# Kernel optimization log

Hardware: AMD Instinct MI355X
Metric: run time of the kernel (lower is better)

## Reference

```python
import jax, jax.numpy as jnp
import numpy as np

F_NODE = 256   # node_feat_size
H      = 256   # hidden_size (must equal F_NODE due to expand using feat_size)
M      = 128   # max_child_num
T      = 4     # edge_type_num
ITERS  = 2     # num_iterations
NSEM   = 57    # Tree.num_sem


def setup_inputs() -> dict:
    key = jax.random.key(0)
    ks = jax.random.split(key, 12)

    def lin(k, fan_in, shape):
        return jax.random.normal(k, shape, jnp.float32) / np.sqrt(fan_in).astype(np.float32)

    return dict(
        parent_feature=jax.random.normal(ks[0], (1, F_NODE), jnp.float32),
        gt_children_code=jax.random.normal(ks[1], (1, 16), jnp.float32),
        gt_num_code=jax.random.normal(ks[2], (1, 10), jnp.float32),
        W_parent=lin(ks[3], F_NODE + 26, (F_NODE + 26, H * M)),
        b_parent=jnp.zeros((H * M,), jnp.float32),
        W_exists=lin(ks[4], H, (H, 1)),
        b_exists=jnp.zeros((1,), jnp.float32),
        W_sem=lin(ks[5], H, (H, NSEM)),
        b_sem=jnp.zeros((NSEM,), jnp.float32),
        W_el=lin(ks[6], 2 * H, (2 * H, H)),
        b_el=jnp.zeros((H,), jnp.float32),
        W_ee=lin(ks[7], H, (T, H)),          # stacked per-type [H,1] heads
        b_ee=jnp.zeros((T,), jnp.float32),
        W_ne=lin(ks[8], 3 * H + T, (ITERS, 3 * H + T, H)),
        b_ne=jnp.zeros((ITERS, H), jnp.float32),
        W_child=lin(ks[9], (ITERS + 1) * H, ((ITERS + 1) * H, H)),
        b_child=jnp.zeros((H,), jnp.float32),
        W_child2=lin(ks[10], H, (H, F_NODE)),
        b_child2=jnp.zeros((F_NODE,), jnp.float32),
    )


def reference(parent_feature, gt_children_code, gt_num_code,
              W_parent, b_parent, W_exists, b_exists, W_sem, b_sem,
              W_el, b_el, W_ee, b_ee, W_ne, b_ne,
              W_child, b_child, W_child2, b_child2):
    B = parent_feature.shape[0]  # == 1 (message passing uses batch index 0 only)

    pf = jnp.concatenate([parent_feature, gt_children_code, gt_num_code], axis=1)
    child_feats = jax.nn.relu(pf @ W_parent + b_parent).reshape(B, M, H)

    child_exists_logits = child_feats @ W_exists + b_exists           # [B,M,1]

    # pairwise edge latents [B,M,M,H]
    pair = jnp.concatenate([
        jnp.broadcast_to(child_feats[:, :, None, :], (B, M, M, H)),
        jnp.broadcast_to(child_feats[:, None, :, :], (B, M, M, H)),
    ], axis=3)
    edge_latents = jax.nn.relu(pair @ W_el + b_el)                    # [B,M,M,H]
    edge_exists_logits = jnp.einsum('bijh,th->bijt', edge_latents, W_ee) + b_ee  # [B,M,M,T]

    # --- masked full candidate edge set (replaces data-dependent torch.nonzero) ---
    ii, jj, tt = jnp.meshgrid(jnp.arange(M), jnp.arange(M), jnp.arange(T), indexing='ij')
    i = ii.reshape(-1)   # [E] source nodes
    j = jj.reshape(-1)
    t = tt.reshape(-1)

    logit_e = edge_exists_logits[0].reshape(-1)                        # [E], same (i,j,t) order
    exists0 = child_exists_logits[0, :, 0] > 0                         # [M]
    mask = (logit_e > 0) & exists0[i] & exists0[j]                     # [E]
    maskf = mask.astype(child_feats.dtype)[:, None]

    edge_feats_mp = edge_latents[0][i, j]                              # [E,H]
    edge_type_logit = jax.nn.one_hot(t, T, dtype=logit_e.dtype) * logit_e[:, None]  # [E,T]
    ef = jnp.concatenate([edge_feats_mp, edge_type_logit], axis=1)     # [E,H+T]

    cf0 = child_feats[0]                                               # [M,H]
    iter_feats = [cf0]
    for it in range(ITERS):
        x = jnp.concatenate([cf0[i], cf0[j], ef], axis=1)              # [E,3H+T]
        msg = jax.nn.relu(x @ W_ne[it] + b_ne[it]) * maskf             # masked msgs are 0
        # scatter_max with zero-initialized out (relu msgs >= 0, matches torch_scatter out=zeros)
        cf0 = jnp.zeros((M, H), msg.dtype).at[i].max(msg)
        iter_feats.append(cf0)

    all_feats = jnp.concatenate(iter_feats, axis=1)                    # [M,(ITERS+1)H]
    h = jax.nn.relu(all_feats @ W_child + b_child)                     # [M,H]
    child_sem_logits = (h @ W_sem + b_sem)[None]                       # [1,M,NSEM]
    child_out = jax.nn.relu(h @ W_child2 + b_child2)[None]             # [1,M,F_NODE]
    return (child_out, child_sem_logits, child_exists_logits, edge_exists_logits)
```

## Files before the change

kernel.cpp:

```cpp
#include <hip/hip_runtime.h>
#include <hip/hip_bf16.h>
#include <stdint.h>


typedef unsigned short ushort_t;
using f32x4 = __attribute__((ext_vector_type(4))) float;
using s16x8 = __attribute__((ext_vector_type(8))) short;

__device__ __forceinline__ ushort_t f2bf(float x) {
  __hip_bfloat16 h = __float2bfloat16(x);
  return *reinterpret_cast<ushort_t*>(&h);
}

__global__ __launch_bounds__(256) void k1_parent(
    const float* __restrict__ p0, const float* __restrict__ p1, const float* __restrict__ p2,
    const float* __restrict__ W, const float* __restrict__ b, float* __restrict__ cf) {
  __shared__ float pfs[282];
  __shared__ f32x4 red[320];
  int tid = threadIdx.x;
  pfs[tid] = p0[tid];
  if (tid < 16) pfs[256 + tid] = p1[tid];
  if (tid < 10) pfs[272 + tid] = p2[tid];
  __syncthreads();
  int c = tid & 7, s = tid >> 3;
  int colg = blockIdx.x * 8 + c;
  const f32x4* W4 = (const f32x4*)W;
  int k0 = (s * 282) >> 5, k1e = ((s + 1) * 282) >> 5;
  f32x4 acc = {0.f, 0.f, 0.f, 0.f};
  #pragma unroll 4
  for (int k = k0; k < k1e; ++k)
    acc += pfs[k] * W4[(size_t)k * 8192 + colg];
  red[s * 8 + c] = acc;
  __syncthreads();
  if (tid < 64) {
    int col = tid & 7, part = tid >> 3;
    f32x4 v = red[(part * 4 + 0) * 8 + col] + red[(part * 4 + 1) * 8 + col]
            + red[(part * 4 + 2) * 8 + col] + red[(part * 4 + 3) * 8 + col];
    red[256 + part * 8 + col] = v;
  }
  __syncthreads();
  if (tid < 8) {
    f32x4 v = red[256 + tid];
    #pragma unroll
    for (int q = 1; q < 8; ++q) v += red[256 + q * 8 + tid];
    v += ((const f32x4*)b)[blockIdx.x * 8 + tid];
    #pragma unroll
    for (int q = 0; q < 4; ++q) v[q] = fmaxf(v[q], 0.f);
    ((f32x4*)cf)[blockIdx.x * 8 + tid] = v;
  }
}

__global__ __launch_bounds__(1024) void ks1(
    const float* __restrict__ cf, const float* __restrict__ Wel,
    const float* __restrict__ Wne, const float* __restrict__ bne,
    const float* __restrict__ Wex, const float* __restrict__ bex,
    float* __restrict__ A, float* __restrict__ B, float* __restrict__ P,
    float* __restrict__ Q, float* __restrict__ ex0, float* __restrict__ exout,
    ushort_t* __restrict__ W3T) {
  __shared__ float c[256];
  __shared__ float redA[1024], redB[1024], redP[1024], redQ[1024];
  __shared__ float wsum[4];
  int tid = threadIdx.x;
  int r = blockIdx.x >> 1, half = blockIdx.x & 1;
  if (tid < 256) c[tid] = cf[r * 256 + tid];
  __syncthreads();
  int cc = tid & 127, s = tid >> 7;
  int col = half * 128 + cc;
  int k0 = s * 32;
  const float* WelB = Wel + 256 * 256;
  float aA = 0.f, aB = 0.f, aP = 0.f, aQ = 0.f;
  #pragma unroll 4
  for (int kk = 0; kk < 32; ++kk) {
    int k = k0 + kk;
    float cv = c[k];
    aA += cv * Wel[k * 256 + col];
    aB += cv * WelB[k * 256 + col];
    aP += cv * Wne[k * 256 + col];
    aQ += cv * Wne[(256 + k) * 256 + col];
  }
  redA[tid] = aA; redB[tid] = aB; redP[tid] = aP; redQ[tid] = aQ;
  float v = (half == 0 && tid < 256) ? c[tid] * Wex[tid] : 0.f;
  #pragma unroll
  for (int off = 32; off; off >>= 1) v += __shfl_xor(v, off);
  if (half == 0 && tid < 256 && (tid & 63) == 0) wsum[tid >> 6] = v;
  __syncthreads();
  if (tid < 128) {
    int cl = half * 128 + tid;
    float a = 0.f, bb = 0.f, pv = bne[cl], qv = 0.f;
    #pragma unroll
    for (int q = 0; q < 8; ++q) {
      a  += redA[q * 128 + tid];
      bb += redB[q * 128 + tid];
      pv += redP[q * 128 + tid];
      qv += redQ[q * 128 + tid];
    }
    A[r * 256 + cl] = a;
    B[r * 256 + cl] = bb;
    P[r * 256 + cl] = pv;
    Q[r * 256 + cl] = qv;
  }
  if (half == 0 && tid == 0) {
    float lg = wsum[0] + wsum[1] + wsum[2] + wsum[3] + bex[0];
    exout[r] = lg;
    ex0[r] = lg > 0.f ? 1.f : 0.f;
  }
  if (tid < 512) {
    int idx = blockIdx.x * 512 + tid;
    int it = idx >> 16, n = (idx >> 8) & 255, k = idx & 255;
    W3T[it * 65536 + n * 256 + (k ^ ((n & 7) << 3))] =
        f2bf(Wne[(size_t)(it * 772 + 512 + k) * 256 + n]);
  }
}

__global__ __launch_bounds__(256) void k3_edge(
    const float* __restrict__ A, const float* __restrict__ B, const float* __restrict__ bel,
    const float* __restrict__ Wee, const float* __restrict__ bee,
    ushort_t* __restrict__ ELbf, float* __restrict__ elog) {
  __shared__ float w4s[4][4][4];
  int tid = threadIdx.x, lane = tid & 63, wid = tid >> 6;
  int p0 = blockIdx.x * 4;
  int i = p0 >> 7;
  float a = A[i * 256 + tid] + bel[tid];
  float we0 = Wee[tid], we1 = Wee[256 + tid], we2 = Wee[512 + tid], we3 = Wee[768 + tid];
  #pragma unroll
  for (int jj = 0; jj < 4; ++jj) {
    int pr = p0 + jj;
    int j = pr & 127;
    float el = fmaxf(a + B[j * 256 + tid], 0.f);
    ELbf[(size_t)pr * 256 + (tid ^ ((pr & 7) << 3))] = f2bf(el);
    float t0 = el * we0, t1 = el * we1, t2 = el * we2, t3 = el * we3;
    #pragma unroll
    for (int off = 32; off; off >>= 1) {
      t0 += __shfl_xor(t0, off);
      t1 += __shfl_xor(t1, off);
      t2 += __shfl_xor(t2, off);
      t3 += __shfl_xor(t3, off);
    }
    if (lane == 0) { w4s[jj][wid][0] = t0; w4s[jj][wid][1] = t1;
                     w4s[jj][wid][2] = t2; w4s[jj][wid][3] = t3; }
  }
  __syncthreads();
  if (tid < 16) {
    int jj = tid >> 2, t = tid & 3;
    float v = w4s[jj][0][t] + w4s[jj][1][t] + w4s[jj][2][t] + w4s[jj][3][t] + bee[t];
    elog[(p0 + jj) * 4 + t] = v;
  }
}

__global__ __launch_bounds__(512) void kf(
    const ushort_t* __restrict__ ELbf, const ushort_t* __restrict__ W3T_it,
    const float* __restrict__ Wne_it, const float* __restrict__ P,
    const float* __restrict__ Q, const float* __restrict__ ex0,
    const float* __restrict__ elog, float* __restrict__ cfn) {
  __shared__ __align__(16) ushort_t lA[128 * 256];
  __shared__ __align__(16) ushort_t lB[128 * 256];
  __shared__ float sl[512];
  __shared__ float se[128];
  __shared__ float red[256];
  int tid = threadIdx.x;
  int i = blockIdx.x >> 1, nh = blockIdx.x & 1;
  if (ex0[i] == 0.f) {
    if (tid < 128) cfn[i * 256 + nh * 128 + tid] = 0.f;
    return;
  }
  int lane = tid & 63, wid = tid >> 6;
  int wr = wid >> 2, wc = wid & 3;
  sl[tid] = elog[i * 512 + tid];
  if (tid < 128) se[tid] = ex0[tid];
  float pv = (tid < 128) ? P[i * 256 + nh * 128 + tid] : 0.f;
  float qv[2][16];
  float w4v[2][4];
  #pragma unroll
  for (int nt = 0; nt < 2; ++nt) {
    int col = nh * 128 + wc * 32 + nt * 16 + (lane & 15);
    #pragma unroll
    for (int t = 0; t < 4; ++t) w4v[nt][t] = Wne_it[(768 + t) * 256 + col];
    #pragma unroll
    for (int mt = 0; mt < 4; ++mt)
      #pragma unroll
      for (int r = 0; r < 4; ++r) {
        int j = wr * 64 + mt * 16 + (lane >> 4) * 4 + r;
        qv[nt][mt * 4 + r] = Q[j * 256 + col];
      }
  }
  #pragma unroll
  for (int rr = 0; rr < 8; ++rr) {
    int c = rr * 8 + wid;
    const ushort_t* sa = ELbf + (size_t)(i * 128) * 256 + c * 512 + lane * 8;
    const ushort_t* sb = W3T_it + (size_t)(nh * 128) * 256 + c * 512 + lane * 8;
    __builtin_amdgcn_global_load_lds((const __attribute__((address_space(1))) void*)sa,
                                     (__attribute__((address_space(3))) void*)(lA + c * 512), 16, 0, 0);
    __builtin_amdgcn_global_load_lds((const __attribute__((address_space(1))) void*)sb,
                                     (__attribute__((address_space(3))) void*)(lB + c * 512), 16, 0, 0);
  }
  __syncthreads();
  f32x4 acc[4][2] = {};
  #pragma unroll
  for (int ks = 0; ks < 8; ++ks) {
    s16x8 af[4], bfr[2];
    #pragma unroll
    for (int mt = 0; mt < 4; ++mt) {
      int row = wr * 64 + mt * 16 + (lane & 15);
      int kl = (ks * 32 + (lane >> 4) * 8) ^ ((row & 7) << 3);
      af[mt] = *reinterpret_cast<const s16x8*>(&lA[row * 256 + kl]);
    }
    #pragma unroll
    for (int nt = 0; nt < 2; ++nt) {
      int n = wc * 32 + nt * 16 + (lane & 15);
      int kl = (ks * 32 + (lane >> 4) * 8) ^ ((n & 7) << 3);
      bfr[nt] = *reinterpret_cast<const s16x8*>(&lB[n * 256 + kl]);
    }
    #pragma unroll
    for (int mt = 0; mt < 4; ++mt)
      #pragma unroll
      for (int nt = 0; nt < 2; ++nt)
        acc[mt][nt] = __builtin_amdgcn_mfma_f32_16x16x32_bf16(af[mt], bfr[nt], acc[mt][nt], 0, 0, 0);
  }
  const float NEG = -3.0e38f;
  #pragma unroll
  for (int nt = 0; nt < 2; ++nt) {
    float mx = NEG;
    #pragma unroll
    for (int mt = 0; mt < 4; ++mt)
      #pragma unroll
      for (int r = 0; r < 4; ++r) {
        int j = wr * 64 + mt * 16 + (lane >> 4) * 4 + r;
        float base = acc[mt][nt][r] + qv[nt][mt * 4 + r];
        if (se[j] > 0.f) {
          float l0 = sl[j * 4 + 0], l1 = sl[j * 4 + 1];
          float l2 = sl[j * 4 + 2], l3 = sl[j * 4 + 3];
          if (l0 > 0.f) mx = fmaxf(mx, base + l0 * w4v[nt][0]);
          if (l1 > 0.f) mx = fmaxf(mx, base + l1 * w4v[nt][1]);
          if (l2 > 0.f) mx = fmaxf(mx, base + l2 * w4v[nt][2]);
          if (l3 > 0.f) mx = fmaxf(mx, base + l3 * w4v[nt][3]);
        }
      }
    mx = fmaxf(mx, __shfl_xor(mx, 16));
    mx = fmaxf(mx, __shfl_xor(mx, 32));
    if (lane < 16) red[wr * 128 + wc * 32 + nt * 16 + lane] = mx;
  }
  __syncthreads();
  if (tid < 128) {
    float m = fmaxf(red[tid], red[128 + tid]);
    cfn[i * 256 + nh * 128 + tid] = fmaxf(pv + m, 0.f);
  }
}

__global__ __launch_bounds__(1024) void kp1(
    const float* __restrict__ cf, const float* __restrict__ Wne_it,
    const float* __restrict__ bne_it, float* __restrict__ P, float* __restrict__ Q) {
  __shared__ float c[256];
  __shared__ float redP[1024], redQ[1024];
  int tid = threadIdx.x;
  int r = blockIdx.x >> 1, half = blockIdx.x & 1;
  if (tid < 256) c[tid] = cf[r * 256 + tid];
  __syncthreads();
  int cc = tid & 127, s = tid >> 7;
  int col = half * 128 + cc;
  int k0 = s * 32;
  float aP = 0.f, aQ = 0.f;
  #pragma unroll 4
  for (int kk = 0; kk < 32; ++kk) {
    int k = k0 + kk;
    float cv = c[k];
    aP += cv * Wne_it[k * 256 + col];
    aQ += cv * Wne_it[(256 + k) * 256 + col];
  }
  redP[tid] = aP; redQ[tid] = aQ;
  __syncthreads();
  if (tid < 128) {
    int cl = half * 128 + tid;
    float pv = bne_it[cl], qv = 0.f;
    #pragma unroll
    for (int q = 0; q < 8; ++q) { pv += redP[q * 128 + tid]; qv += redQ[q * 128 + tid]; }
    P[r * 256 + cl] = pv;
    Q[r * 256 + cl] = qv;
  }
}

__global__ __launch_bounds__(1024) void k6_final(
    const float* __restrict__ cf0, const float* __restrict__ cf1, const float* __restrict__ cf2,
    const float* __restrict__ Wc, const float* __restrict__ bc,
    const float* __restrict__ Wsem, const float* __restrict__ bsem,
    const float* __restrict__ W2, const float* __restrict__ b2,
    float* __restrict__ out) {
  __shared__ float af[768];
  __shared__ float red[1024];
  __shared__ float hrow[256];
  __shared__ float redS[8 * 57];
  int tid = threadIdx.x;
  int m = blockIdx.x >> 1, half = blockIdx.x & 1;
  if (tid < 768) {
    af[tid] = tid < 256 ? cf0[m * 256 + tid]
            : tid < 512 ? cf1[m * 256 + tid - 256]
                        : cf2[m * 256 + tid - 512];
  }
  __syncthreads();
  {
    int cc = tid & 255, s = tid >> 8;
    float acc = 0.f;
    #pragma unroll 4
    for (int kk = 0; kk < 192; ++kk) {
      int k = s * 192 + kk;
      acc += af[k] * Wc[k * 256 + cc];
    }
    red[tid] = acc;
  }
  __syncthreads();
  if (tid < 256) {
    float v = bc[tid] + red[tid] + red[256 + tid] + red[512 + tid] + red[768 + tid];
    hrow[tid] = fmaxf(v, 0.f);
  }
  __syncthreads();
  int cc = tid & 127, s = tid >> 7;
  int col = half * 128 + cc;
  {
    float acc = 0.f;
    #pragma unroll 4
    for (int kk = 0; kk < 32; ++kk) {
      int k = s * 32 + kk;
      acc += hrow[k] * W2[k * 256 + col];
    }
    red[tid] = acc;
    if (half == 0 && cc < 57) {
      float accs = 0.f;
      #pragma unroll 4
      for (int kk = 0; kk < 32; ++kk) {
        int k = s * 32 + kk;
        accs += hrow[k] * Wsem[k * 57 + cc];
      }
      redS[s * 57 + cc] = accs;
    }
  }
  __syncthreads();
  if (tid < 128) {
    float v = b2[half * 128 + tid];
    #pragma unroll
    for (int q = 0; q < 8; ++q) v += red[q * 128 + tid];
    out[m * 256 + half * 128 + tid] = fmaxf(v, 0.f);
  }
  if (half == 0 && tid < 57) {
    float v = bsem[tid];
    #pragma unroll
    for (int q = 0; q < 8; ++q) v += redS[q * 57 + tid];
    out[32768 + m * 57 + tid] = v;
  }
}

extern "C" void kernel_launch(void* const* d_in, const int* in_sizes, int n_in,
                              void* d_out, int out_size, void* d_ws, size_t ws_size,
                              hipStream_t stream) {
  const float* p0  = (const float*)d_in[0];
  const float* p1  = (const float*)d_in[1];
  const float* p2  = (const float*)d_in[2];
  const float* Wp  = (const float*)d_in[3];
  const float* bp  = (const float*)d_in[4];
  const float* Wex = (const float*)d_in[5];
  const float* bex = (const float*)d_in[6];
  const float* Wsm = (const float*)d_in[7];
  const float* bsm = (const float*)d_in[8];
  const float* Wel = (const float*)d_in[9];
  const float* bel = (const float*)d_in[10];
  const float* Wee = (const float*)d_in[11];
  const float* bee = (const float*)d_in[12];
  const float* Wne = (const float*)d_in[13];
  const float* bne = (const float*)d_in[14];
  const float* Wc  = (const float*)d_in[15];
  const float* bc  = (const float*)d_in[16];
  const float* W2  = (const float*)d_in[17];
  const float* b2  = (const float*)d_in[18];
  float* out = (float*)d_out;

  char* ws = (char*)d_ws;
  float*    cf0  = (float*)(ws + 0);
  float*    cf1  = (float*)(ws + 131072);
  float*    cf2  = (float*)(ws + 262144);
  float*    Ab   = (float*)(ws + 393216);
  float*    Bb   = (float*)(ws + 524288);
  float*    Pb   = (float*)(ws + 655360);
  float*    Qb   = (float*)(ws + 786432);
  float*    Pb2  = (float*)(ws + 917504);
  float*    Qb2  = (float*)(ws + 1048576);
  float*    ex0  = (float*)(ws + 1179648);
  ushort_t* W3T  = (ushort_t*)(ws + 1310720);
  ushort_t* ELbf = (ushort_t*)(ws + 2097152);

  float* out_ex = out + 40064;
  float* out_el = out + 40192;

  const float* Wne1 = Wne + 772 * 256;

  k1_parent<<<1024, 256, 0, stream>>>(p0, p1, p2, Wp, bp, cf0);
  ks1<<<256, 1024, 0, stream>>>(cf0, Wel, Wne, bne, Wex, bex,
                                Ab, Bb, Pb, Qb, ex0, out_ex, W3T);
  k3_edge<<<4096, 256, 0, stream>>>(Ab, Bb, bel, Wee, bee, ELbf, out_el);
  kf<<<256, 512, 0, stream>>>(ELbf, W3T, Wne, Pb, Qb, ex0, out_el, cf1);
  kp1<<<256, 1024, 0, stream>>>(cf1, Wne1, bne + 256, Pb2, Qb2);
  kf<<<256, 512, 0, stream>>>(ELbf, W3T + 65536, Wne1, Pb2, Qb2, ex0, out_el, cf2);
  k6_final<<<256, 1024, 0, stream>>>(cf0, cf1, cf2, Wc, bc, Wsm, bsm, W2, b2, out);
}
```

Baseline: 187.8 us.

## Fuse edge-latent computation into message-passing GEMM kernel, recompute per iteration

Drops the separate edge kernel and its bf16 edge-latent buffer in global memory. Each message-passing block now builds its 128x256 edge-latent tile directly in LDS from the A row, the B matrix and the bias. The first iteration's instance also computes the edge-type logits and writes them out. This removes a launch and a write/read round trip of the pairwise tensor, at the cost of recomputing the tile in both iterations and in both column-half blocks, plus extra LDS and global reads of B per block.

```diff
diff --git a/kernel.cpp b/kernel.cpp
--- a/kernel.cpp
+++ b/kernel.cpp
@@ -112,88 +112,107 @@
   }
 }
 
-__global__ __launch_bounds__(256) void k3_edge(
-    const float* __restrict__ A, const float* __restrict__ B, const float* __restrict__ bel,
-    const float* __restrict__ Wee, const float* __restrict__ bee,
-    ushort_t* __restrict__ ELbf, float* __restrict__ elog) {
-  __shared__ float w4s[4][4][4];
-  int tid = threadIdx.x, lane = tid & 63, wid = tid >> 6;
-  int p0 = blockIdx.x * 4;
-  int i = p0 >> 7;
-  float a = A[i * 256 + tid] + bel[tid];
-  float we0 = Wee[tid], we1 = Wee[256 + tid], we2 = Wee[512 + tid], we3 = Wee[768 + tid];
-  #pragma unroll
-  for (int jj = 0; jj < 4; ++jj) {
-    int pr = p0 + jj;
-    int j = pr & 127;
-    float el = fmaxf(a + B[j * 256 + tid], 0.f);
-    ELbf[(size_t)pr * 256 + (tid ^ ((pr & 7) << 3))] = f2bf(el);
-    float t0 = el * we0, t1 = el * we1, t2 = el * we2, t3 = el * we3;
-    #pragma unroll
-    for (int off = 32; off; off >>= 1) {
-      t0 += __shfl_xor(t0, off);
-      t1 += __shfl_xor(t1, off);
-      t2 += __shfl_xor(t2, off);
-      t3 += __shfl_xor(t3, off);
-    }
-    if (lane == 0) { w4s[jj][wid][0] = t0; w4s[jj][wid][1] = t1;
-                     w4s[jj][wid][2] = t2; w4s[jj][wid][3] = t3; }
-  }
-  __syncthreads();
-  if (tid < 16) {
-    int jj = tid >> 2, t = tid & 3;
-    float v = w4s[jj][0][t] + w4s[jj][1][t] + w4s[jj][2][t] + w4s[jj][3][t] + bee[t];
-    elog[(p0 + jj) * 4 + t] = v;
-  }
-}
-
-__global__ __launch_bounds__(512) void kf(
-    const ushort_t* __restrict__ ELbf, const ushort_t* __restrict__ W3T_it,
+template<int WRITE_EL>
+__global__ __launch_bounds__(512) void kf2(
+    const float* __restrict__ A, const float* __restrict__ Bm,
+    const float* __restrict__ bel, const float* __restrict__ Wee,
+    const float* __restrict__ bee, const ushort_t* __restrict__ W3T_it,
     const float* __restrict__ Wne_it, const float* __restrict__ P,
     const float* __restrict__ Q, const float* __restrict__ ex0,
-    const float* __restrict__ elog, float* __restrict__ cfn) {
+    float* __restrict__ elog, float* __restrict__ cfn) {
   __shared__ __align__(16) ushort_t lA[128 * 256];
   __shared__ __align__(16) ushort_t lB[128 * 256];
+  __shared__ float arow[256], belr[256];
+  __shared__ float weer[1024];
   __shared__ float sl[512];
   __shared__ float se[128];
   __shared__ float red[256];
   int tid = threadIdx.x;
   int i = blockIdx.x >> 1, nh = blockIdx.x & 1;
-  if (ex0[i] == 0.f) {
+  bool alive = ex0[i] != 0.f;
+  if (!alive && (WRITE_EL == 0 || nh == 1)) {
     if (tid < 128) cfn[i * 256 + nh * 128 + tid] = 0.f;
     return;
   }
   int lane = tid & 63, wid = tid >> 6;
   int wr = wid >> 2, wc = wid & 3;
-  sl[tid] = elog[i * 512 + tid];
+  if (alive) {
+    #pragma unroll
+    for (int rr = 0; rr < 8; ++rr) {
+      int ch = rr * 8 + wid;
+      const ushort_t* sb = W3T_it + (size_t)(nh * 128) * 256 + ch * 512 + lane * 8;
+      __builtin_amdgcn_global_load_lds((const __attribute__((address_space(1))) void*)sb,
+                                       (__attribute__((address_space(3))) void*)(lB + ch * 512), 16, 0, 0);
+    }
+  }
+  if (tid < 256) { arow[tid] = A[i * 256 + tid]; belr[tid] = bel[tid]; }
   if (tid < 128) se[tid] = ex0[tid];
-  float pv = (tid < 128) ? P[i * 256 + nh * 128 + tid] : 0.f;
+  if (WRITE_EL) { weer[tid] = Wee[tid]; weer[512 + tid] = Wee[512 + tid]; }
+  else sl[tid] = elog[i * 512 + tid];
+  float pv = 0.f;
   float qv[2][16];
   float w4v[2][4];
+  if (alive) {
+    pv = (tid < 128) ? P[i * 256 + nh * 128 + tid] : 0.f;
+    #pragma unroll
+    for (int nt = 0; nt < 2; ++nt) {
+      int col = nh * 128 + wc * 32 + nt * 16 + (lane & 15);
+      #pragma unroll
+      for (int t = 0; t < 4; ++t) w4v[nt][t] = Wne_it[(768 + t) * 256 + col];
+      #pragma unroll
+      for (int mt = 0; mt < 4; ++mt)
+        #pragma unroll
+        for (int r = 0; r < 4; ++r)
+          qv[nt][mt * 4 + r] = Q[(wr * 64 + mt * 16 + (lane >> 4) * 4 + r) * 256 + col];
+    }
+  }
+  __syncthreads();
+  int j = tid >> 2, q = tid & 3;
+  int sw = (j & 7) << 3;
+  float lg0 = 0.f, lg1 = 0.f, lg2 = 0.f, lg3 = 0.f;
+  const float* Bj = Bm + j * 256;
   #pragma unroll
-  for (int nt = 0; nt < 2; ++nt) {
-    int col = nh * 128 + wc * 32 + nt * 16 + (lane & 15);
-    #pragma unroll
-    for (int t = 0; t < 4; ++t) w4v[nt][t] = Wne_it[(768 + t) * 256 + col];
-    #pragma unroll
-    for (int mt = 0; mt < 4; ++mt)
+  for (int ch = 0; ch < 8; ++ch) {
+    int c0 = q * 64 + ch * 8;
+    float el[8];
+    #pragma unroll
+    for (int e = 0; e < 8; ++e)
+      el[e] = fmaxf(arow[c0 + e] + Bj[c0 + e] + belr[c0 + e], 0.f);
+    if (WRITE_EL) {
       #pragma unroll
-      for (int r = 0; r < 4; ++r) {
-        int j = wr * 64 + mt * 16 + (lane >> 4) * 4 + r;
-        qv[nt][mt * 4 + r] = Q[j * 256 + col];
+      for (int e = 0; e < 8; ++e) {
+        lg0 += el[e] * weer[c0 + e];
+        lg1 += el[e] * weer[256 + c0 + e];
+        lg2 += el[e] * weer[512 + c0 + e];
+        lg3 += el[e] * weer[768 + c0 + e];
       }
-  }
-  #pragma unroll
-  for (int rr = 0; rr < 8; ++rr) {
-    int c = rr * 8 + wid;
-    const ushort_t* sa = ELbf + (size_t)(i * 128) * 256 + c * 512 + lane * 8;
-    const ushort_t* sb = W3T_it + (size_t)(nh * 128) * 256 + c * 512 + lane * 8;
-    __builtin_amdgcn_global_load_lds((const __attribute__((address_space(1))) void*)sa,
-                                     (__attribute__((address_space(3))) void*)(lA + c * 512), 16, 0, 0);
-    __builtin_amdgcn_global_load_lds((const __attribute__((address_space(1))) void*)sb,
-                                     (__attribute__((address_space(3))) void*)(lB + c * 512), 16, 0, 0);
-  }
-  __syncthreads();
+    }
+    s16x8 sv;
+    #pragma unroll
+    for (int e = 0; e < 8; ++e) sv[e] = (short)f2bf(el[e]);
+    *reinterpret_cast<s16x8*>(&lA[j * 256 + (c0 ^ sw)]) = sv;
+  }
+  if (WRITE_EL) {
+    lg0 += __shfl_xor(lg0, 1); lg0 += __shfl_xor(lg0, 2);
+    lg1 += __shfl_xor(lg1, 1); lg1 += __shfl_xor(lg1, 2);
+    lg2 += __shfl_xor(lg2, 1); lg2 += __shfl_xor(lg2, 2);
+    lg3 += __shfl_xor(lg3, 1); lg3 += __shfl_xor(lg3, 2);
+    if (q == 0) {
+      float v0 = lg0 + bee[0], v1 = lg1 + bee[1], v2 = lg2 + bee[2], v3 = lg3 + bee[3];
+      sl[j * 4 + 0] = v0; sl[j * 4 + 1] = v1; sl[j * 4 + 2] = v2; sl[j * 4 + 3] = v3;
+      if (nh == 0) {
+        elog[(i * 128 + j) * 4 + 0] = v0;
+        elog[(i * 128 + j) * 4 + 1] = v1;
+        elog[(i * 128 + j) * 4 + 2] = v2;
+        elog[(i * 128 + j) * 4 + 3] = v3;
+      }
+    }
+  }
+  __syncthreads();
+  if (!alive) {
+    if (tid < 128) cfn[i * 256 + tid] = 0.f;
+    return;
+  }
   f32x4 acc[4][2] = {};
   #pragma unroll
   for (int ks = 0; ks < 8; ++ks) {
@@ -224,11 +243,11 @@
     for (int mt = 0; mt < 4; ++mt)
       #pragma unroll
       for (int r = 0; r < 4; ++r) {
-        int j = wr * 64 + mt * 16 + (lane >> 4) * 4 + r;
+        int jj = wr * 64 + mt * 16 + (lane >> 4) * 4 + r;
         float base = acc[mt][nt][r] + qv[nt][mt * 4 + r];
-        if (se[j] > 0.f) {
-          float l0 = sl[j * 4 + 0], l1 = sl[j * 4 + 1];
-          float l2 = sl[j * 4 + 2], l3 = sl[j * 4 + 3];
+        if (se[jj] > 0.f) {
+          float l0 = sl[jj * 4 + 0], l1 = sl[jj * 4 + 1];
+          float l2 = sl[jj * 4 + 2], l3 = sl[jj * 4 + 3];
           if (l0 > 0.f) mx = fmaxf(mx, base + l0 * w4v[nt][0]);
           if (l1 > 0.f) mx = fmaxf(mx, base + l1 * w4v[nt][1]);
           if (l2 > 0.f) mx = fmaxf(mx, base + l2 * w4v[nt][2]);
@@ -383,7 +402,6 @@
   float*    Qb2  = (float*)(ws + 1048576);
   float*    ex0  = (float*)(ws + 1179648);
   ushort_t* W3T  = (ushort_t*)(ws + 1310720);
-  ushort_t* ELbf = (ushort_t*)(ws + 2097152);
 
   float* out_ex = out + 40064;
   float* out_el = out + 40192;
@@ -393,9 +411,10 @@
   k1_parent<<<1024, 256, 0, stream>>>(p0, p1, p2, Wp, bp, cf0);
   ks1<<<256, 1024, 0, stream>>>(cf0, Wel, Wne, bne, Wex, bex,
                                 Ab, Bb, Pb, Qb, ex0, out_ex, W3T);
-  k3_edge<<<4096, 256, 0, stream>>>(Ab, Bb, bel, Wee, bee, ELbf, out_el);
-  kf<<<256, 512, 0, stream>>>(ELbf, W3T, Wne, Pb, Qb, ex0, out_el, cf1);
+  kf2<1><<<256, 512, 0, stream>>>(Ab, Bb, bel, Wee, bee, W3T, Wne,
+                                  Pb, Qb, ex0, out_el, cf1);
   kp1<<<256, 1024, 0, stream>>>(cf1, Wne1, bne + 256, Pb2, Qb2);
-  kf<<<256, 512, 0, stream>>>(ELbf, W3T + 65536, Wne1, Pb2, Qb2, ex0, out_el, cf2);
+  kf2<0><<<256, 512, 0, stream>>>(Ab, Bb, bel, Wee, bee, W3T + 65536, Wne1,
+                                  Pb2, Qb2, ex0, out_el, cf2);
   k6_final<<<256, 1024, 0, stream>>>(cf0, cf1, cf2, Wc, bc, Wsm, bsm, W2, b2, out);
 }
```

After: 179.4 us. 1.05x faster.
